# Optimization experiments

Hardware: AMD Instinct MI355X
Metric: run time of the kernel (lower is better)

Reference implementation:

```python
import jax, jax.numpy as jnp
import numpy as np

F_E, F_XT, F_XS, F_U = 10, 5, 10, 10
N_S, N_T, E, B = 100000, 100000, 4000000, 64
D1 = F_E + F_XT           # 15
D2 = F_XS + 1 + 4 * D1 + F_U  # 81


def setup_inputs() -> dict:
    key = jax.random.key(0)
    ks = jax.random.split(key, 16)
    inp = {
        'x_s': jax.random.normal(ks[0], (N_S, F_XS), jnp.float32),
        'x_t': jax.random.normal(ks[1], (N_T, F_XT), jnp.float32),
        'edge_attr': jax.random.normal(ks[2], (E, F_E), jnp.float32),
        'u': jax.random.normal(ks[3], (B, F_U), jnp.float32),
        'edge_index': jax.random.randint(ks[4], (2, E), 0, N_S, jnp.int32).astype(jnp.int64),
        'batch_s': jax.random.randint(ks[5], (N_S,), 0, B, jnp.int32).astype(jnp.int64),
        # node_mlp_1: Linear(15,15) -> LeakyReLU(0.1) -> Linear(15,15)
        'w1a': jax.random.normal(ks[6], (D1, D1), jnp.float32) / np.sqrt(D1),
        'b1a': jnp.zeros((D1,), jnp.float32),
        'w2a': jax.random.normal(ks[7], (D1, D1), jnp.float32) / np.sqrt(D1),
        'b2a': jnp.zeros((D1,), jnp.float32),
        # node_mlp_2: Linear(81,10) -> LeakyReLU(0.1) -> Linear(10,10)
        'w1b': jax.random.normal(ks[8], (D2, F_XS), jnp.float32) / np.sqrt(D2),
        'b1b': jnp.zeros((F_XS,), jnp.float32),
        'w2b': jax.random.normal(ks[9], (F_XS, F_XS), jnp.float32) / np.sqrt(F_XS),
        'b2b': jnp.zeros((F_XS,), jnp.float32),
    }
    return inp


def reference(x_s, x_t, edge_attr, u, edge_index, batch_s,
              w1a, b1a, w2a, b2a, w1b, b1b, w2b, b2b):
    src, tgt = edge_index[0], edge_index[1]
    n = x_s.shape[0]

    # message MLP over gathered target features + edge attrs: [E, 15]
    msg = jnp.concatenate([x_t[tgt], edge_attr], axis=1)
    msg = jax.nn.leaky_relu(msg @ w1a + b1a, 0.1) @ w2a + b2a

    seg = lambda v: jax.ops.segment_sum(v, src, num_segments=n)
    count = seg(jnp.ones((msg.shape[0], 1), msg.dtype))         # [N_s, 1]
    denom = jnp.maximum(count, 1.0)                             # torch_scatter mean: /max(count,1)
    mean = seg(msg) / denom                                     # [N_s, 15]
    mean2 = seg(msg * msg) / denom
    var = jax.nn.relu(mean2 - mean * mean)
    std = jnp.sqrt(var + 1e-6)
    d = msg - mean[src]
    d3 = d * d * d
    skew = (seg(d3) / denom) / (std ** 3)
    kurt = (seg(d3 * d) / denom) / (std ** 4)

    h = jnp.concatenate([x_s, count, mean, std, skew, kurt, u[batch_s]], axis=1)  # [N_s, 81]
    return jax.nn.leaky_relu(h @ w1b + b1b, 0.1) @ w2b + b2b
```

## Files before the change

kernel.cpp:

```cpp
#include <hip/hip_runtime.h>
#include <hip/hip_fp16.h>
#include <math.h>

#define NBMAX    1024
#define NSUPMAX  32
#define C2       1024
#define RD       9
#define CH4      512
#define SLOTS    61

__device__ __forceinline__ float leaky(float x) { return fmaxf(x, 0.1f * x); }
__device__ __forceinline__ unsigned int packh(float a, float b) {
    return (unsigned int)__half_as_ushort(__float2half(a)) |
           ((unsigned int)__half_as_ushort(__float2half(b)) << 16);
}

__global__ __launch_bounds__(1024, 8) void binmlp_kernel(
    const int* __restrict__ edge_index, const float* __restrict__ x_t,
    const float* __restrict__ edge_attr,
    const float* __restrict__ w1a, const float* __restrict__ b1a,
    const float* __restrict__ w2a, const float* __restrict__ b2a,
    int* __restrict__ acur, unsigned int* __restrict__ A,
    int E, int g0s, int g1s, int capS)
{
    __shared__ unsigned int ys[C2 * RD];
    __shared__ unsigned short s_sp[C2];
    __shared__ int shist[NSUPMAX], sexcl[NSUPMAX], sgof[NSUPMAX];
    __shared__ int s_total;
    __shared__ float sw1[240], sw2[240], sb1[16], sb2[16];
    int tid = threadIdx.x;

    if (tid < 240)      { int r = tid >> 4, c = tid & 15; sw1[tid] = (c < 15) ? w1a[r * 15 + c] : 0.f; }
    else if (tid < 480) { int i = tid - 240; int r = i >> 4, c = i & 15; sw2[i] = (c < 15) ? w2a[r * 15 + c] : 0.f; }
    else if (tid < 495) sb1[tid - 480] = b1a[tid - 480];
    else if (tid < 510) sb2[tid - 495] = b2a[tid - 495];
    if (tid >= 512 && tid < 512 + NSUPMAX) shist[tid - 512] = 0;
    __syncthreads();

    int ei = blockIdx.x * C2 + tid;
    int su = -1, rank = 0;
    unsigned int us[8];
    if (ei < E) {
        int s = edge_index[ei];
        int sup = s >> 12;
        if (sup >= g0s && sup < g1s) {
            su = sup - g0s;
            int tgt = edge_index[E + ei];

            float in0[15];
            const float* xt = x_t + (size_t)tgt * 5;
#pragma unroll
            for (int r = 0; r < 5; r++) in0[r] = xt[r];
            const float2* ea = (const float2*)(edge_attr + (size_t)ei * 10);
#pragma unroll
            for (int r = 0; r < 5; r++) { float2 t2 = ea[r]; in0[5 + 2 * r] = t2.x; in0[6 + 2 * r] = t2.y; }

            float h[15];
#pragma unroll
            for (int j = 0; j < 15; j++) h[j] = sb1[j];
#pragma unroll
            for (int ii = 0; ii < 15; ii++)
#pragma unroll
                for (int j = 0; j < 15; j++) h[j] = fmaf(in0[ii], sw1[ii * 16 + j], h[j]);
#pragma unroll
            for (int j = 0; j < 15; j++) h[j] = leaky(h[j]);

            float y[15];
#pragma unroll
            for (int j = 0; j < 15; j++) y[j] = sb2[j];
#pragma unroll
            for (int ii = 0; ii < 15; ii++)
#pragma unroll
                for (int j = 0; j < 15; j++) y[j] = fmaf(h[ii], sw2[ii * 16 + j], y[j]);

#pragma unroll
            for (int j = 0; j < 7; j++) us[j] = packh(y[2 * j], y[2 * j + 1]);
            us[7] = (unsigned int)__half_as_ushort(__float2half(y[14])) |
                    ((unsigned int)(s & 4095) << 16);

            rank = atomicAdd(&shist[su], 1);
        }
    }
    __syncthreads();

    if (tid < 64) {
        int v = (tid < NSUPMAX) ? shist[tid] : 0;
        int inc = v;
#pragma unroll
        for (int d = 1; d < 64; d <<= 1) { int m = __shfl_up(inc, d); if (tid >= d) inc += m; }
        if (tid < NSUPMAX) {
            sexcl[tid] = inc - v;
            if (v) sgof[tid] = atomicAdd(&acur[g0s + tid], v) - (inc - v);
        }
        if (tid == 63) s_total = inc;
    }
    __syncthreads();

    if (su >= 0) {
        int p = sexcl[su] + rank;
        s_sp[p] = (unsigned short)su;
        unsigned int* yr = &ys[p * RD];
#pragma unroll
        for (int j = 0; j < 8; j++) yr[j] = us[j];
    }
    __syncthreads();

    int total = s_total;
    for (int i = tid; i < total; i += 1024) {
        unsigned int v[8];
        const unsigned int* yr = &ys[i * RD];
#pragma unroll
        for (int j = 0; j < 8; j++) v[j] = yr[j];
        int sp = s_sp[i];
        int o = sgof[sp] + i;
        if ((unsigned)o < (unsigned)capS) {
            size_t rec = (size_t)sp * capS + o;
            uint4* dst = (uint4*)(A + rec * 8);
            dst[0] = make_uint4(v[0], v[1], v[2], v[3]);
            dst[1] = make_uint4(v[4], v[5], v[6], v[7]);
        }
    }
}

__global__ __launch_bounds__(1024, 8) void rebin_kernel(
    const unsigned int* __restrict__ A, const int* __restrict__ acur,
    int* __restrict__ bcur2, unsigned int* __restrict__ B,
    int g0s, int capS, int cps, int capB)
{
    int srel = blockIdx.x / cps;
    int c    = blockIdx.x - srel * cps;
    int s    = g0s + srel;
    int nsup = min(acur[s], capS);
    int off  = c * C2;
    if (off >= nsup) return;

    __shared__ unsigned int ys[C2 * RD];
    __shared__ unsigned short s_sb[C2];
    __shared__ int shist[32], sexcl[32], sgof[32];
    int tid = threadIdx.x;
    if (tid < 32) shist[tid] = 0;
    int n = min(C2, nsup - off);
    __syncthreads();

    size_t abase = (size_t)srel * capS + off;
    uint4 r0, r1;
    int sb = -1, rk = 0;
    if (tid < n) {
        const uint4* ap = (const uint4*)(A + (abase + tid) * 8);
        r0 = ap[0]; r1 = ap[1];
        sb = (int)((r1.w >> 23) & 31);
        rk = atomicAdd(&shist[sb], 1);
    }
    __syncthreads();

    if (tid < 64) {
        int v = (tid < 32) ? shist[tid] : 0;
        int inc = v;
#pragma unroll
        for (int d = 1; d < 64; d <<= 1) { int m = __shfl_up(inc, d); if (tid >= d) inc += m; }
        if (tid < 32) {
            sexcl[tid] = inc - v;
            if (v) sgof[tid] = atomicAdd(&bcur2[(s << 5) + tid], v) - (inc - v);
        }
    }
    __syncthreads();

    if (sb >= 0) {
        int p = sexcl[sb] + rk;
        s_sb[p] = (unsigned short)sb;
        unsigned int* yr = &ys[p * RD];
        yr[0] = r0.x; yr[1] = r0.y; yr[2] = r0.z; yr[3] = r0.w;
        yr[4] = r1.x; yr[5] = r1.y; yr[6] = r1.z; yr[7] = r1.w;
    }
    __syncthreads();

    int fbrel0 = srel << 5;
    for (int i = tid; i < n; i += 1024) {
        unsigned int v[8];
        const unsigned int* yr = &ys[i * RD];
#pragma unroll
        for (int j = 0; j < 8; j++) v[j] = yr[j];
        int b = s_sb[i];
        int o = sgof[b] + i;
        if ((unsigned)o < (unsigned)capB) {
            size_t rec = (size_t)(fbrel0 + b) * capB + o;
            uint4* dst = (uint4*)(B + rec * 8);
            dst[0] = make_uint4(v[0], v[1], v[2], v[3]);
            dst[1] = make_uint4(v[4], v[5], v[6], v[7]);
        }
    }
}

__global__ __launch_bounds__(512, 2) void moment_kernel(
    const unsigned int* __restrict__ B, const int* __restrict__ bcur2,
    const float* __restrict__ x_s, const float* __restrict__ u,
    const int* __restrict__ batch_s,
    const float* __restrict__ w1b, const float* __restrict__ b1b,
    const float* __restrict__ w2b, const float* __restrict__ b2b,
    float* __restrict__ out, int N, int fb_lo, int capB)
{
    __shared__ unsigned int uys[CH4 * RD];
    __shared__ float accs[128 * SLOTS];
    __shared__ int   shist[128];
    __shared__ int   sstart[129];
    __shared__ float tb1[16], tb2[16];
    int tid = threadIdx.x;
    int fb = fb_lo + blockIdx.x;
    int node0 = fb << 7;
    if (node0 >= N) return;

    if (tid < 10) { tb1[tid] = b1b[tid]; tb2[tid] = b2b[tid]; }
    for (int i = tid; i < 128 * SLOTS; i += 512) accs[i] = 0.f;
    if (tid < 128) shist[tid] = 0;

    int cnt_fb = min(bcur2[fb], capB);
    const unsigned int* Bb = B + (size_t)(fb - fb_lo) * capB * 8;

    int g = tid >> 4, f = tid & 15;
    int dwo = f >> 1, sh = (f & 1) * 16;
    __syncthreads();

    uint4 r0, r1;
    int nid = -1;
    {
        int m0 = min(CH4, cnt_fb);
        if (tid < m0) {
            const uint4* rp = (const uint4*)(Bb + (size_t)tid * 8);
            r0 = rp[0]; r1 = rp[1];
            nid = (int)((r1.w >> 16) & 127);
        }
    }

    for (int e0 = 0; e0 < cnt_fb; e0 += CH4) {
        int rank = 0;
        if (nid >= 0) rank = atomicAdd(&shist[nid], 1);
        __syncthreads();

        if (tid < 64) {
            int carry = 0;
            for (int base = 0; base < 128; base += 64) {
                int i = base + tid;
                int v = shist[i];
                int inc = v;
#pragma unroll
                for (int d = 1; d < 64; d <<= 1) { int mm = __shfl_up(inc, d); if (tid >= d) inc += mm; }
                sstart[i] = inc - v + carry;
                carry += __shfl(inc, 63);
            }
            if (tid == 63) sstart[128] = carry;
        }
        __syncthreads();

        if (nid >= 0) {
            int p = sstart[nid] + rank;
            unsigned int* yr = &uys[p * RD];
            yr[0] = r0.x; yr[1] = r0.y; yr[2] = r0.z; yr[3] = r0.w;
            yr[4] = r1.x; yr[5] = r1.y; yr[6] = r1.z; yr[7] = r1.w;
        }
        __syncthreads();

        int nnid = -1;
        uint4 n0, n1;
        {
            int mn = min(CH4, cnt_fb - (e0 + CH4));
            if (tid < mn) {
                const uint4* rp = (const uint4*)(Bb + (size_t)(e0 + CH4 + tid) * 8);
                n0 = rp[0]; n1 = rp[1];
                nnid = (int)((n1.w >> 16) & 127);
            }
        }

        for (int nd = g; nd < 128; nd += 32) {
            int st = sstart[nd], en = sstart[nd + 1];
            if (en > st) {
                float s1 = 0.f, s2 = 0.f, s3 = 0.f, s4 = 0.f;
                for (int k = st; k < en; k++) {
                    unsigned int uw = uys[k * RD + dwo];
                    float y = __half2float(__ushort_as_half((unsigned short)((uw >> sh) & 0xFFFF)));
                    float y2 = y * y;
                    s1 += y; s2 += y2; s3 += y2 * y; s4 += y2 * y2;
                }
                int ab = nd * SLOTS;
                if (f < 15) {
                    accs[ab + f]      += s1;
                    accs[ab + 15 + f] += s2;
                    accs[ab + 30 + f] += s3;
                    accs[ab + 45 + f] += s4;
                } else {
                    accs[ab + 60] += (float)(en - st);
                }
            }
        }
        if (tid < 128) shist[tid] = 0;
        __syncthreads();

        r0 = n0; r1 = n1; nid = nnid;
    }

    float* fys = reinterpret_cast<float*>(uys);
    float* tw1 = fys;
    float* tw2 = fys + 810;
    float* o1s = fys + 910;
    for (int i = tid; i < 810; i += 512) tw1[i] = w1b[i];
    for (int i = tid; i < 100; i += 512) tw2[i] = w2b[i];

    for (int idx = tid; idx < 128 * 16; idx += 512) {
        int ff = idx & 15, nd = idx >> 4;
        if (ff < 15 && node0 + nd < N) {
            int ab = nd * SLOTS;
            float cf  = accs[ab + 60];
            float inv = 1.0f / fmaxf(cf, 1.0f);
            float m1 = accs[ab + ff]      * inv;
            float m2 = accs[ab + 15 + ff] * inv;
            float m3 = accs[ab + 30 + ff] * inv;
            float m4 = accs[ab + 45 + ff] * inv;
            float var = fmaxf(m2 - m1 * m1, 0.0f);
            float sd  = sqrtf(var + 1e-6f);
            float m1sq = m1 * m1;
            float c3 = m3 - 3.0f * m1 * m2 + 2.0f * m1sq * m1;
            float c4 = m4 - 4.0f * m1 * m3 + 6.0f * m1sq * m2 - 3.0f * m1sq * m1sq;
            float is = 1.0f / sd, is2 = is * is;
            accs[ab + ff]      = m1;
            accs[ab + 15 + ff] = sd;
            accs[ab + 30 + ff] = c3 * is2 * is;
            accs[ab + 45 + ff] = c4 * is2 * is2;
        }
    }
    __syncthreads();

    for (int idx = tid; idx < 128 * 10; idx += 512) {
        int nd = idx / 10, k = idx - nd * 10;
        int node = node0 + nd;
        if (node >= N) continue;
        int ab = nd * SLOTS;
        float acc = tb1[k];
        const float* xs = x_s + (size_t)node * 10;
#pragma unroll
        for (int j = 0; j < 10; j++) acc = fmaf(xs[j], tw1[j * 10 + k], acc);
        acc = fmaf(accs[ab + 60], tw1[100 + k], acc);
#pragma unroll
        for (int ff = 0; ff < 15; ff++) acc = fmaf(accs[ab + ff],      tw1[(11 + ff) * 10 + k], acc);
#pragma unroll
        for (int ff = 0; ff < 15; ff++) acc = fmaf(accs[ab + 15 + ff], tw1[(26 + ff) * 10 + k], acc);
#pragma unroll
        for (int ff = 0; ff < 15; ff++) acc = fmaf(accs[ab + 30 + ff], tw1[(41 + ff) * 10 + k], acc);
#pragma unroll
        for (int ff = 0; ff < 15; ff++) acc = fmaf(accs[ab + 45 + ff], tw1[(56 + ff) * 10 + k], acc);
        const float* uu = u + (size_t)batch_s[node] * 10;
#pragma unroll
        for (int j = 0; j < 10; j++) acc = fmaf(uu[j], tw1[(71 + j) * 10 + k], acc);
        o1s[idx] = leaky(acc);
    }
    __syncthreads();
    for (int idx = tid; idx < 128 * 10; idx += 512) {
        int nd = idx / 10, k = idx - nd * 10;
        int node = node0 + nd;
        if (node >= N) continue;
        float acc = tb2[k];
#pragma unroll
        for (int mm = 0; mm < 10; mm++) acc = fmaf(o1s[nd * 10 + mm], tw2[mm * 10 + k], acc);
        out[(size_t)node * 10 + k] = acc;
    }
}

extern "C" void kernel_launch(void* const* d_in, const int* in_sizes, int n_in,
                              void* d_out, int out_size, void* d_ws, size_t ws_size,
                              hipStream_t stream)
{
    const float* x_s       = (const float*)d_in[0];
    const float* x_t       = (const float*)d_in[1];
    const float* edge_attr = (const float*)d_in[2];
    const float* u         = (const float*)d_in[3];
    const int*   edge_index= (const int*)d_in[4];
    const int*   batch_s   = (const int*)d_in[5];
    const float* w1a = (const float*)d_in[6];
    const float* b1a = (const float*)d_in[7];
    const float* w2a = (const float*)d_in[8];
    const float* b2a = (const float*)d_in[9];
    const float* w1b = (const float*)d_in[10];
    const float* b1b = (const float*)d_in[11];
    const float* w2b = (const float*)d_in[12];
    const float* b2b = (const float*)d_in[13];

    int N = in_sizes[0] / 10;
    int E = in_sizes[2] / 10;
    int NB   = (N + 127) >> 7;
    int NSUP = (NB + 31) >> 5;

    long epS = ((long)E * 4096 + N - 1) / N;
    long sS  = (long)(sqrt((double)epS) + 1.0);
    long capSl = epS + 4 * sS + 512;
    int capS = (int)(((capSl + C2 - 1) / C2) * C2);
    long epB = ((long)E * 128 + N - 1) / N;
    long sB  = (long)(sqrt((double)epB) + 1.0);
    int capB = (int)(((epB + 5 * sB + 64 + 15) / 16) * 16);

    char* p = (char*)d_ws;
    auto take = [&](size_t bytes) { char* r = p; p += (bytes + 255) & ~(size_t)255; return r; };
    int* acur  = (int*)take((size_t)NSUPMAX * 4);
    int* bcur2 = (int*)take((size_t)NBMAX * 4);
    size_t head  = (size_t)(p - (char*)d_ws);
    size_t avail = (ws_size > head) ? ws_size - head : 0;
    size_t perS  = ((size_t)capS + (size_t)32 * (size_t)capB) * 32;
    int NSsw = (int)(avail / perS);
    if (NSsw < 1) NSsw = 1;
    if (NSsw > NSUP) NSsw = NSUP;
    unsigned int* A = (unsigned int*)take((size_t)NSsw * (size_t)capS * 32);
    unsigned int* B = (unsigned int*)take((size_t)NSsw * 32 * (size_t)capB * 32);

    hipMemsetAsync(acur,  0, (size_t)NSUPMAX * 4, stream);
    hipMemsetAsync(bcur2, 0, (size_t)NBMAX * 4, stream);

    int cps = capS / C2;
    int k2grid = (E + C2 - 1) / C2;
    for (int g0 = 0; g0 < NSUP; g0 += NSsw) {
        int g1 = g0 + NSsw; if (g1 > NSUP) g1 = NSUP;
        binmlp_kernel<<<k2grid, 1024, 0, stream>>>(
            edge_index, x_t, edge_attr, w1a, b1a, w2a, b2a,
            acur, A, E, g0, g1, capS);
        rebin_kernel<<<(g1 - g0) * cps, 1024, 0, stream>>>(
            A, acur, bcur2, B, g0, capS, cps, capB);
        int fb_lo = g0 << 5;
        int fb_hi = g1 << 5; if (fb_hi > NB) fb_hi = NB;
        moment_kernel<<<fb_hi - fb_lo, 512, 0, stream>>>(
            B, bcur2, x_s, u, batch_s,
            w1b, b1b, w2b, b2b, (float*)d_out, N, fb_lo, capB);
    }
}
```

Baseline: 502.8 us.

## Replace shared-memory prefix scans with per-wave redundant scans and shrink block sizes

After: 519.5 us. 3.3% more time.

```diff
diff --git a/kernel.cpp b/kernel.cpp
--- a/kernel.cpp
+++ b/kernel.cpp
@@ -4,7 +4,8 @@
 
 #define NBMAX    1024
 #define NSUPMAX  32
-#define C2       1024
+#define C2B      512
+#define C3       1024
 #define RD       9
 #define CH4      512
 #define SLOTS    61
@@ -14,8 +15,14 @@
     return (unsigned int)__half_as_ushort(__float2half(a)) |
            ((unsigned int)__half_as_ushort(__float2half(b)) << 16);
 }
-
-__global__ __launch_bounds__(1024, 8) void binmlp_kernel(
+__device__ __forceinline__ int wincl(int v, int lane) {
+    int inc = v;
+#pragma unroll
+    for (int d = 1; d < 64; d <<= 1) { int m = __shfl_up(inc, d); if (lane >= d) inc += m; }
+    return inc;
+}
+
+__global__ __launch_bounds__(512, 4) void binmlp_kernel(
     const int* __restrict__ edge_index, const float* __restrict__ x_t,
     const float* __restrict__ edge_attr,
     const float* __restrict__ w1a, const float* __restrict__ b1a,
@@ -23,21 +30,23 @@
     int* __restrict__ acur, unsigned int* __restrict__ A,
     int E, int g0s, int g1s, int capS)
 {
-    __shared__ unsigned int ys[C2 * RD];
-    __shared__ unsigned short s_sp[C2];
-    __shared__ int shist[NSUPMAX], sexcl[NSUPMAX], sgof[NSUPMAX];
+    __shared__ unsigned int ys[C2B * RD];
+    __shared__ unsigned short s_sp[C2B];
+    __shared__ int shist[NSUPMAX], sgof[NSUPMAX];
     __shared__ int s_total;
     __shared__ float sw1[240], sw2[240], sb1[16], sb2[16];
-    int tid = threadIdx.x;
-
-    if (tid < 240)      { int r = tid >> 4, c = tid & 15; sw1[tid] = (c < 15) ? w1a[r * 15 + c] : 0.f; }
-    else if (tid < 480) { int i = tid - 240; int r = i >> 4, c = i & 15; sw2[i] = (c < 15) ? w2a[r * 15 + c] : 0.f; }
-    else if (tid < 495) sb1[tid - 480] = b1a[tid - 480];
-    else if (tid < 510) sb2[tid - 495] = b2a[tid - 495];
-    if (tid >= 512 && tid < 512 + NSUPMAX) shist[tid - 512] = 0;
-    __syncthreads();
-
-    int ei = blockIdx.x * C2 + tid;
+    int tid = threadIdx.x, lane = tid & 63;
+
+    for (int i = tid; i < 240; i += 512) {
+        int r = i >> 4, c = i & 15;
+        sw1[i] = (c < 15) ? w1a[r * 15 + c] : 0.f;
+        sw2[i] = (c < 15) ? w2a[r * 15 + c] : 0.f;
+    }
+    if (tid < 15) { sb1[tid] = b1a[tid]; sb2[tid] = b2a[tid]; }
+    if (tid < NSUPMAX) shist[tid] = 0;
+    __syncthreads();
+
+    int ei = blockIdx.x * C2B + tid;
     int su = -1, rank = 0;
     unsigned int us[8];
     if (ei < E) {
@@ -83,36 +92,33 @@
     }
     __syncthreads();
 
-    if (tid < 64) {
-        int v = (tid < NSUPMAX) ? shist[tid] : 0;
-        int inc = v;
-#pragma unroll
-        for (int d = 1; d < 64; d <<= 1) { int m = __shfl_up(inc, d); if (tid >= d) inc += m; }
+    {
+        int v = (lane < NSUPMAX) ? shist[lane] : 0;
+        int inc = wincl(v, lane);
+        int exc = inc - v;
+        int pexc = __shfl(exc, su & 31);
         if (tid < NSUPMAX) {
-            sexcl[tid] = inc - v;
-            if (v) sgof[tid] = atomicAdd(&acur[g0s + tid], v) - (inc - v);
+            if (v) sgof[tid] = atomicAdd(&acur[g0s + tid], v) - exc;
         }
         if (tid == 63) s_total = inc;
-    }
-    __syncthreads();
-
-    if (su >= 0) {
-        int p = sexcl[su] + rank;
-        s_sp[p] = (unsigned short)su;
-        unsigned int* yr = &ys[p * RD];
-#pragma unroll
-        for (int j = 0; j < 8; j++) yr[j] = us[j];
+        if (su >= 0) {
+            int p = pexc + rank;
+            s_sp[p] = (unsigned short)su;
+            unsigned int* yr = &ys[p * RD];
+#pragma unroll
+            for (int j = 0; j < 8; j++) yr[j] = us[j];
+        }
     }
     __syncthreads();
 
     int total = s_total;
-    for (int i = tid; i < total; i += 1024) {
+    if (tid < total) {
         unsigned int v[8];
-        const unsigned int* yr = &ys[i * RD];
+        const unsigned int* yr = &ys[tid * RD];
 #pragma unroll
         for (int j = 0; j < 8; j++) v[j] = yr[j];
-        int sp = s_sp[i];
-        int o = sgof[sp] + i;
+        int sp = s_sp[tid];
+        int o = sgof[sp] + tid;
         if ((unsigned)o < (unsigned)capS) {
             size_t rec = (size_t)sp * capS + o;
             uint4* dst = (uint4*)(A + rec * 8);
@@ -122,7 +128,7 @@
     }
 }
 
-__global__ __launch_bounds__(1024, 8) void rebin_kernel(
+__global__ __launch_bounds__(512, 4) void rebin_kernel(
     const unsigned int* __restrict__ A, const int* __restrict__ acur,
     int* __restrict__ bcur2, unsigned int* __restrict__ B,
     int g0s, int capS, int cps, int capB)
@@ -131,51 +137,62 @@
     int c    = blockIdx.x - srel * cps;
     int s    = g0s + srel;
     int nsup = min(acur[s], capS);
-    int off  = c * C2;
+    int off  = c * C3;
     if (off >= nsup) return;
 
-    __shared__ unsigned int ys[C2 * RD];
-    __shared__ unsigned short s_sb[C2];
-    __shared__ int shist[32], sexcl[32], sgof[32];
-    int tid = threadIdx.x;
+    __shared__ unsigned int ys[C3 * RD];
+    __shared__ unsigned short s_sb[C3];
+    __shared__ int shist[32], sgof[32];
+    int tid = threadIdx.x, lane = tid & 63;
     if (tid < 32) shist[tid] = 0;
-    int n = min(C2, nsup - off);
+    int n = min(C3, nsup - off);
     __syncthreads();
 
     size_t abase = (size_t)srel * capS + off;
-    uint4 r0, r1;
-    int sb = -1, rk = 0;
+    uint4 r0a, r1a, r0b, r1b;
+    int sb0 = -1, sb1v = -1, rk0 = 0, rk1 = 0;
     if (tid < n) {
         const uint4* ap = (const uint4*)(A + (abase + tid) * 8);
-        r0 = ap[0]; r1 = ap[1];
-        sb = (int)((r1.w >> 23) & 31);
-        rk = atomicAdd(&shist[sb], 1);
-    }
-    __syncthreads();
-
-    if (tid < 64) {
-        int v = (tid < 32) ? shist[tid] : 0;
-        int inc = v;
-#pragma unroll
-        for (int d = 1; d < 64; d <<= 1) { int m = __shfl_up(inc, d); if (tid >= d) inc += m; }
+        r0a = ap[0]; r1a = ap[1];
+        sb0 = (int)((r1a.w >> 23) & 31);
+        rk0 = atomicAdd(&shist[sb0], 1);
+    }
+    if (tid + 512 < n) {
+        const uint4* ap = (const uint4*)(A + (abase + tid + 512) * 8);
+        r0b = ap[0]; r1b = ap[1];
+        sb1v = (int)((r1b.w >> 23) & 31);
+        rk1 = atomicAdd(&shist[sb1v], 1);
+    }
+    __syncthreads();
+
+    {
+        int v = (lane < 32) ? shist[lane] : 0;
+        int inc = wincl(v, lane);
+        int exc = inc - v;
+        int ex0 = __shfl(exc, sb0 & 31);
+        int ex1 = __shfl(exc, sb1v & 31);
         if (tid < 32) {
-            sexcl[tid] = inc - v;
-            if (v) sgof[tid] = atomicAdd(&bcur2[(s << 5) + tid], v) - (inc - v);
-        }
-    }
-    __syncthreads();
-
-    if (sb >= 0) {
-        int p = sexcl[sb] + rk;
-        s_sb[p] = (unsigned short)sb;
-        unsigned int* yr = &ys[p * RD];
-        yr[0] = r0.x; yr[1] = r0.y; yr[2] = r0.z; yr[3] = r0.w;
-        yr[4] = r1.x; yr[5] = r1.y; yr[6] = r1.z; yr[7] = r1.w;
+            if (v) sgof[tid] = atomicAdd(&bcur2[(s << 5) + tid], v) - exc;
+        }
+        if (sb0 >= 0) {
+            int p = ex0 + rk0;
+            s_sb[p] = (unsigned short)sb0;
+            unsigned int* yr = &ys[p * RD];
+            yr[0] = r0a.x; yr[1] = r0a.y; yr[2] = r0a.z; yr[3] = r0a.w;
+            yr[4] = r1a.x; yr[5] = r1a.y; yr[6] = r1a.z; yr[7] = r1a.w;
+        }
+        if (sb1v >= 0) {
+            int p = ex1 + rk1;
+            s_sb[p] = (unsigned short)sb1v;
+            unsigned int* yr = &ys[p * RD];
+            yr[0] = r0b.x; yr[1] = r0b.y; yr[2] = r0b.z; yr[3] = r0b.w;
+            yr[4] = r1b.x; yr[5] = r1b.y; yr[6] = r1b.z; yr[7] = r1b.w;
+        }
     }
     __syncthreads();
 
     int fbrel0 = srel << 5;
-    for (int i = tid; i < n; i += 1024) {
+    for (int i = tid; i < n; i += 512) {
         unsigned int v[8];
         const unsigned int* yr = &ys[i * RD];
 #pragma unroll
@@ -202,9 +219,8 @@
     __shared__ unsigned int uys[CH4 * RD];
     __shared__ float accs[128 * SLOTS];
     __shared__ int   shist[128];
-    __shared__ int   sstart[129];
     __shared__ float tb1[16], tb2[16];
-    int tid = threadIdx.x;
+    int tid = threadIdx.x, lane = tid & 63;
     int fb = fb_lo + blockIdx.x;
     int node0 = fb << 7;
     if (node0 >= N) return;
@@ -236,23 +252,18 @@
         if (nid >= 0) rank = atomicAdd(&shist[nid], 1);
         __syncthreads();
 
-        if (tid < 64) {
-            int carry = 0;
-            for (int base = 0; base < 128; base += 64) {
-                int i = base + tid;
-                int v = shist[i];
-                int inc = v;
-#pragma unroll
-                for (int d = 1; d < 64; d <<= 1) { int mm = __shfl_up(inc, d); if (tid >= d) inc += mm; }
-                sstart[i] = inc - v + carry;
-                carry += __shfl(inc, 63);
-            }
-            if (tid == 63) sstart[128] = carry;
-        }
-        __syncthreads();
-
+        int va = shist[lane], vb = shist[lane + 64];
+        int ia = wincl(va, lane);
+        int Ta = __shfl(ia, 63);
+        int ib = wincl(vb, lane);
+        int ea = ia - va;
+        int eb = Ta + ib - vb;
+        int tot = Ta + __shfl(ib, 63);
+        int nidc = nid & 127;
+        int exA = __shfl(ea, nidc & 63);
+        int exB = __shfl(eb, nidc & 63);
         if (nid >= 0) {
-            int p = sstart[nid] + rank;
+            int p = ((nidc < 64) ? exA : exB) + rank;
             unsigned int* yr = &uys[p * RD];
             yr[0] = r0.x; yr[1] = r0.y; yr[2] = r0.z; yr[3] = r0.w;
             yr[4] = r1.x; yr[5] = r1.y; yr[6] = r1.z; yr[7] = r1.w;
@@ -271,7 +282,13 @@
         }
 
         for (int nd = g; nd < 128; nd += 32) {
-            int st = sstart[nd], en = sstart[nd + 1];
+            int sA = __shfl(ea, nd & 63);
+            int sB = __shfl(eb, nd & 63);
+            int st = (nd < 64) ? sA : sB;
+            int nd1 = nd + 1;
+            int tA = __shfl(ea, nd1 & 63);
+            int tB = __shfl(eb, nd1 & 63);
+            int en = (nd1 >= 128) ? tot : ((nd1 < 64) ? tA : tB);
             if (en > st) {
                 float s1 = 0.f, s2 = 0.f, s3 = 0.f, s4 = 0.f;
                 for (int k = st; k < en; k++) {
@@ -390,7 +407,7 @@
     long epS = ((long)E * 4096 + N - 1) / N;
     long sS  = (long)(sqrt((double)epS) + 1.0);
     long capSl = epS + 4 * sS + 512;
-    int capS = (int)(((capSl + C2 - 1) / C2) * C2);
+    int capS = (int)(((capSl + C3 - 1) / C3) * C3);
     long epB = ((long)E * 128 + N - 1) / N;
     long sB  = (long)(sqrt((double)epB) + 1.0);
     int capB = (int)(((epB + 5 * sB + 64 + 15) / 16) * 16);
@@ -411,14 +428,14 @@
     hipMemsetAsync(acur,  0, (size_t)NSUPMAX * 4, stream);
     hipMemsetAsync(bcur2, 0, (size_t)NBMAX * 4, stream);
 
-    int cps = capS / C2;
-    int k2grid = (E + C2 - 1) / C2;
+    int cps = capS / C3;
+    int k2grid = (E + C2B - 1) / C2B;
     for (int g0 = 0; g0 < NSUP; g0 += NSsw) {
         int g1 = g0 + NSsw; if (g1 > NSUP) g1 = NSUP;
-        binmlp_kernel<<<k2grid, 1024, 0, stream>>>(
+        binmlp_kernel<<<k2grid, 512, 0, stream>>>(
             edge_index, x_t, edge_attr, w1a, b1a, w2a, b2a,
             acur, A, E, g0, g1, capS);
-        rebin_kernel<<<(g1 - g0) * cps, 1024, 0, stream>>>(
+        rebin_kernel<<<(g1 - g0) * cps, 512, 0, stream>>>(
             A, acur, bcur2, B, g0, capS, cps, capB);
         int fb_lo = g0 << 5;
         int fb_hi = g1 << 5; if (fb_hi > NB) fb_hi = NB;
```
